# Optimization experiments

Hardware: AMD Instinct MI355X
Metric: run time of the kernel (lower is better)

Reference implementation:

```python
import jax, jax.numpy as jnp
import numpy as np

INPUT_SIZE = 768
HIDDEN = 384


def _gru_dir(x, W_ih, W_hh, b_ih, b_hh, reverse):
    """Single-direction GRU, torch gate order (r, z, n).
    x: [B, S, D] -> outputs [B, S, H]."""
    B = x.shape[0]
    H = W_hh.shape[1]
    # Precompute input projections for all timesteps: [B, S, 3H] -> [S, B, 3H]
    xw = jnp.swapaxes(x @ W_ih.T + b_ih, 0, 1)

    def step(h, xw_t):
        gh = h @ W_hh.T + b_hh
        xr, xz, xn = jnp.split(xw_t, 3, axis=-1)
        hr, hz, hn = jnp.split(gh, 3, axis=-1)
        r = jax.nn.sigmoid(xr + hr)
        z = jax.nn.sigmoid(xz + hz)
        n = jnp.tanh(xn + r * hn)
        h_new = (1.0 - z) * n + z * h
        return h_new, h_new

    h0 = jnp.zeros((B, H), dtype=x.dtype)
    _, hs = jax.lax.scan(step, h0, xw, reverse=reverse)  # [S, B, H]
    return jnp.swapaxes(hs, 0, 1)


def setup_inputs() -> dict:
    key = jax.random.key(0)
    ks = jax.random.split(key, 12)
    B, S, D, H = 32, 512, INPUT_SIZE, HIDDEN
    s_ih = 1.0 / np.sqrt(H)
    u = lambda k, shape: jax.random.uniform(k, shape, jnp.float32, -s_ih, s_ih)
    inp = {
        "ip": jax.random.normal(ks[0], (B, S, D), jnp.float32),
        # forward-direction GRU params
        "W_ih_f": u(ks[1], (3 * H, D)),
        "W_hh_f": u(ks[2], (3 * H, H)),
        "b_ih_f": u(ks[3], (3 * H,)),
        "b_hh_f": u(ks[4], (3 * H,)),
        # backward-direction GRU params
        "W_ih_b": u(ks[5], (3 * H, D)),
        "W_hh_b": u(ks[6], (3 * H, H)),
        "b_ih_b": u(ks[7], (3 * H,)),
        "b_hh_b": u(ks[8], (3 * H,)),
        # sentence attention params (input_dim = 2H)
        "W_attn": u(ks[9], (2 * H, 2 * H)),
        "b_attn": u(ks[10], (2 * H,)),
        "context": jax.random.normal(ks[11], (2 * H,), jnp.float32) * 0.05,
    }
    return inp


def reference(ip, W_ih_f, W_hh_f, b_ih_f, b_hh_f,
              W_ih_b, W_hh_b, b_ih_b, b_hh_b,
              W_attn, b_attn, context):
    # BiGRU encode: concat forward & backward hidden states -> [B, S, 2H]
    h_f = _gru_dir(ip, W_ih_f, W_hh_f, b_ih_f, b_hh_f, reverse=False)
    h_b = _gru_dir(ip, W_ih_b, W_hh_b, b_ih_b, b_hh_b, reverse=True)
    out = jnp.concatenate([h_f, h_b], axis=-1)
    # Additive attention pooling over sentences
    scores = jnp.tanh(out @ W_attn.T + b_attn) @ context  # [B, S]
    attn = jax.nn.softmax(scores, axis=1)
    doc_embeds = jnp.einsum("bs,bsd->bd", attn, out)  # [B, 2H]
    return doc_embeds
```

## Files before the change

kernel.cpp:

```cpp
#include <hip/hip_runtime.h>
#include <hip/hip_fp16.h>

typedef _Float16 half2_t __attribute__((ext_vector_type(2)));
typedef _Float16 half4_t __attribute__((ext_vector_type(4)));
typedef _Float16 half8_t __attribute__((ext_vector_type(8)));
typedef float floatx4 __attribute__((ext_vector_type(4)));

#define B_   32
#define S_   512
#define D_   768
#define H_   384
#define H3_  1152
#define M_   (B_*S_)
#define N2_  (2*H3_)
#define TWOH_ 768
#define NWG_DIR 6
#define JSPAN 64

__device__ __forceinline__ int4 load16_cc(const void* p) {
  int4 r;
  unsigned long long a = (unsigned long long)p;
  asm volatile("global_load_dwordx4 %0, %1, off sc0 sc1\n\t"
               "s_waitcnt vmcnt(0)"
               : "=v"(r) : "v"(a) : "memory");
  return r;
}
__device__ __forceinline__ void load16_cc3(const void* p0, const void* p1, const void* p2,
                                           int4& v0, int4& v1, int4& v2) {
  unsigned long long a0 = (unsigned long long)p0;
  unsigned long long a1 = (unsigned long long)p1;
  unsigned long long a2 = (unsigned long long)p2;
  asm volatile("global_load_dwordx4 %0, %3, off sc0 sc1\n\t"
               "global_load_dwordx4 %1, %4, off sc0 sc1\n\t"
               "global_load_dwordx4 %2, %5, off sc0 sc1\n\t"
               "s_waitcnt vmcnt(0)"
               : "=&v"(v0), "=&v"(v1), "=&v"(v2)
               : "v"(a0), "v"(a1), "v"(a2) : "memory");
}
__device__ __forceinline__ void store8_cc(void* p, int2 v) {
  unsigned long long a = (unsigned long long)p;
  asm volatile("global_store_dwordx2 %0, %1, off sc0 sc1"
               :: "v"(a), "v"(v) : "memory");
}
__device__ __forceinline__ void wait_vm0() {
  asm volatile("s_waitcnt vmcnt(0)" ::: "memory");
}

__global__ void cvt_f32_f16_kernel(const float* __restrict__ src,
                                   _Float16* __restrict__ dst, int n4) {
  int i = blockIdx.x * blockDim.x + threadIdx.x;
  if (i >= n4) return;
  float4 v = ((const float4*)src)[i];
  half4_t h = {(_Float16)v.x, (_Float16)v.y, (_Float16)v.z, (_Float16)v.w};
  ((half4_t*)dst)[i] = h;
}

__global__ __launch_bounds__(256) void gemm_xw_kernel(
    const _Float16* __restrict__ A, const _Float16* __restrict__ Bm,
    const float* __restrict__ bias_f, const float* __restrict__ bias_b,
    _Float16* __restrict__ xw) {
  __shared__ _Float16 As[64][40];
  __shared__ _Float16 Bs[64][40];
  const int m0 = blockIdx.x * 64, n0 = blockIdx.y * 64;
  const int tid = threadIdx.x, lane = tid & 63, w = tid >> 6;
  const int wm = w >> 1, wn = w & 1;
  const int q = lane >> 4, c = lane & 15;
  floatx4 acc[2][2] = {};

  const int t = tid & 127;
  const int srow = t >> 1, skh = (t & 1) * 16;
  const _Float16* gsrc =
      (tid < 128 ? A + (size_t)(m0 + srow) * D_ : Bm + (size_t)(n0 + srow) * D_) + skh;
  _Float16* ldst = (tid < 128) ? &As[srow][skh] : &Bs[srow][skh];

  for (int k0 = 0; k0 < D_; k0 += 32) {
    half8_t v0 = *(const half8_t*)(gsrc + k0);
    half8_t v1 = *(const half8_t*)(gsrc + k0 + 8);
    __syncthreads();
    *(half8_t*)ldst = v0;
    *(half8_t*)(ldst + 8) = v1;
    __syncthreads();
    half8_t a0 = *(const half8_t*)&As[wm * 32 + c][q * 8];
    half8_t a1 = *(const half8_t*)&As[wm * 32 + 16 + c][q * 8];
    half8_t b0 = *(const half8_t*)&Bs[wn * 32 + c][q * 8];
    half8_t b1 = *(const half8_t*)&Bs[wn * 32 + 16 + c][q * 8];
    acc[0][0] = __builtin_amdgcn_mfma_f32_16x16x32_f16(a0, b0, acc[0][0], 0, 0, 0);
    acc[0][1] = __builtin_amdgcn_mfma_f32_16x16x32_f16(a0, b1, acc[0][1], 0, 0, 0);
    acc[1][0] = __builtin_amdgcn_mfma_f32_16x16x32_f16(a1, b0, acc[1][0], 0, 0, 0);
    acc[1][1] = __builtin_amdgcn_mfma_f32_16x16x32_f16(a1, b1, acc[1][1], 0, 0, 0);
  }
  for (int mi = 0; mi < 2; ++mi)
    for (int ni = 0; ni < 2; ++ni)
      for (int r = 0; r < 4; ++r) {
        int m = m0 + wm * 32 + mi * 16 + q * 4 + r;
        int n = n0 + wn * 32 + ni * 16 + c;
        int dir = n >= H3_;
        int nn = n - dir * H3_;
        float bv = dir ? bias_b[nn] : bias_f[nn];
        float vv = acc[mi][ni][r] + bv;
        int s = m & (S_ - 1), bb = m >> 9;
        xw[(((size_t)dir * S_ + s) * B_ + bb) * H3_ + nn] = (_Float16)vv;
      }
}

__global__ __launch_bounds__(512, 2) void gru_mfma_kernel(
    const _Float16* __restrict__ xw,
    const _Float16* __restrict__ Whh,
    const float* __restrict__ bhh_f, const float* __restrict__ bhh_b,
    _Float16* __restrict__ hglob,
    _Float16* __restrict__ out16,
    int* __restrict__ bar) {
  const int wg = blockIdx.x;
  const int dir = wg / NWG_DIR;
  const int wgj = wg % NWG_DIR;
  const int j0w = wgj * JSPAN;
  const int tid = threadIdx.x, lane = tid & 63, w = tid >> 6;
  const int bt = w & 1, jt = w >> 1;
  const int c = lane & 15, q = lane >> 4;

  __shared__ __align__(16) _Float16 hS[32 * 392];
  __shared__ __align__(16) float ghS[3 * 32 * 68];

  half8_t bfr[3][12];
  {
    const int jglob = j0w + jt * 16 + c;
#pragma unroll
    for (int g = 0; g < 3; ++g) {
      const _Float16* wp = Whh + ((size_t)dir * H3_ + g * H_ + jglob) * H_ + q * 8;
#pragma unroll
      for (int kt = 0; kt < 12; ++kt) bfr[g][kt] = *(const half8_t*)(wp + kt * 32);
    }
  }
  const float* bhh = dir ? bhh_b : bhh_f;
  const int gb = tid >> 4, jq = tid & 15;
  const int jg4 = j0w + jq * 4;
  float br[4], bz[4], bn[4], hc[4];
#pragma unroll
  for (int i = 0; i < 4; ++i) {
    br[i] = bhh[jg4 + i];
    bz[i] = bhh[H_ + jg4 + i];
    bn[i] = bhh[2 * H_ + jg4 + i];
    hc[i] = 0.f;
  }
  int* flg = bar + dir * 256;

  for (int step = 0; step < S_; ++step) {
    const int t = dir ? (S_ - 1 - step) : step;
    const int par = step & 1;

    const _Float16* xp = xw + (((size_t)dir * S_ + t) * B_ + gb) * H3_ + jg4;
    half4_t xr4 = *(const half4_t*)(xp);
    half4_t xz4 = *(const half4_t*)(xp + H_);
    half4_t xn4 = *(const half4_t*)(xp + 2 * H_);

    if (step > 0 && w == 0) {
      int v;
      do {
        v = (lane < NWG_DIR)
                ? __hip_atomic_load(&flg[lane * 16], __ATOMIC_RELAXED,
                                    __HIP_MEMORY_SCOPE_AGENT)
                : 0x7fffffff;
      } while (!__all(v >= step));
    }
    __syncthreads();

    {
      const _Float16* hb = hglob + ((size_t)dir * 2 + par) * B_ * H_;
      int g0 = tid, g1 = tid + 512, g2 = tid + 1024;
      int4 v0, v1, v2;
      load16_cc3(hb + (g0 / 48) * H_ + (g0 % 48) * 8,
                 hb + (g1 / 48) * H_ + (g1 % 48) * 8,
                 hb + (g2 / 48) * H_ + (g2 % 48) * 8, v0, v1, v2);
      *(int4*)&hS[(g0 / 48) * 392 + (g0 % 48) * 8] = v0;
      *(int4*)&hS[(g1 / 48) * 392 + (g1 % 48) * 8] = v1;
      *(int4*)&hS[(g2 / 48) * 392 + (g2 % 48) * 8] = v2;
    }
    __syncthreads();

    floatx4 a0 = {}, a1 = {}, a2 = {};
    {
      const _Float16* hrow = &hS[(bt * 16 + c) * 392 + q * 8];
#pragma unroll
      for (int kt = 0; kt < 12; ++kt) {
        half8_t af = *(const half8_t*)(hrow + kt * 32);
        a0 = __builtin_amdgcn_mfma_f32_16x16x32_f16(af, bfr[0][kt], a0, 0, 0, 0);
        a1 = __builtin_amdgcn_mfma_f32_16x16x32_f16(af, bfr[1][kt], a1, 0, 0, 0);
        a2 = __builtin_amdgcn_mfma_f32_16x16x32_f16(af, bfr[2][kt], a2, 0, 0, 0);
      }
    }
#pragma unroll
    for (int r = 0; r < 4; ++r) {
      int brow = bt * 16 + q * 4 + r;
      ghS[(0 * 32 + brow) * 68 + jt * 16 + c] = a0[r];
      ghS[(1 * 32 + brow) * 68 + jt * 16 + c] = a1[r];
      ghS[(2 * 32 + brow) * 68 + jt * 16 + c] = a2[r];
    }
    __syncthreads();

    floatx4 arv = *(floatx4*)&ghS[(0 * 32 + gb) * 68 + jq * 4];
    floatx4 azv = *(floatx4*)&ghS[(1 * 32 + gb) * 68 + jq * 4];
    floatx4 anv = *(floatx4*)&ghS[(2 * 32 + gb) * 68 + jq * 4];
    half4_t hh;
#pragma unroll
    for (int i = 0; i < 4; ++i) {
      float rr = 1.f / (1.f + __expf(-((float)xr4[i] + arv[i] + br[i])));
      float zz = 1.f / (1.f + __expf(-((float)xz4[i] + azv[i] + bz[i])));
      float u = (float)xn4[i] + rr * (anv[i] + bn[i]);
      float e = __expf(-2.f * u);
      float nv = (1.f - e) / (1.f + e);
      hc[i] = (1.f - zz) * nv + zz * hc[i];
      hh[i] = (_Float16)hc[i];
    }
    store8_cc(hglob + (((size_t)dir * 2 + (par ^ 1)) * B_ + gb) * H_ + jg4,
              __builtin_bit_cast(int2, hh));
    wait_vm0();
    __syncthreads();
    if (tid == 0)
      __hip_atomic_store(&flg[wgj * 16], step + 1, __ATOMIC_RELAXED,
                         __HIP_MEMORY_SCOPE_AGENT);
    *(half4_t*)&out16[((size_t)gb * S_ + t) * TWOH_ + dir * H_ + jg4] = hh;
  }
}

__global__ __launch_bounds__(256) void attn_score_kernel(
    const _Float16* __restrict__ A ,
    const _Float16* __restrict__ Bm ,
    const float* __restrict__ b_attn, const float* __restrict__ ctx,
    float* __restrict__ scores) {
  __shared__ _Float16 As[64][40];
  __shared__ _Float16 Bs[64][40];
  const int m0 = blockIdx.x * 64, n0 = blockIdx.y * 64;
  const int tid = threadIdx.x, lane = tid & 63, w = tid >> 6;
  const int wm = w >> 1, wn = w & 1;
  const int q = lane >> 4, c = lane & 15;
  floatx4 acc[2][2] = {};

  const int t = tid & 127;
  const int srow = t >> 1, skh = (t & 1) * 16;
  const _Float16* gsrc =
      (tid < 128 ? A + (size_t)(m0 + srow) * D_ : Bm + (size_t)(n0 + srow) * D_) + skh;
  _Float16* ldst = (tid < 128) ? &As[srow][skh] : &Bs[srow][skh];

  for (int k0 = 0; k0 < D_; k0 += 32) {
    half8_t v0 = *(const half8_t*)(gsrc + k0);
    half8_t v1 = *(const half8_t*)(gsrc + k0 + 8);
    __syncthreads();
    *(half8_t*)ldst = v0;
    *(half8_t*)(ldst + 8) = v1;
    __syncthreads();
    half8_t a0 = *(const half8_t*)&As[wm * 32 + c][q * 8];
    half8_t a1 = *(const half8_t*)&As[wm * 32 + 16 + c][q * 8];
    half8_t b0 = *(const half8_t*)&Bs[wn * 32 + c][q * 8];
    half8_t b1 = *(const half8_t*)&Bs[wn * 32 + 16 + c][q * 8];
    acc[0][0] = __builtin_amdgcn_mfma_f32_16x16x32_f16(a0, b0, acc[0][0], 0, 0, 0);
    acc[0][1] = __builtin_amdgcn_mfma_f32_16x16x32_f16(a0, b1, acc[0][1], 0, 0, 0);
    acc[1][0] = __builtin_amdgcn_mfma_f32_16x16x32_f16(a1, b0, acc[1][0], 0, 0, 0);
    acc[1][1] = __builtin_amdgcn_mfma_f32_16x16x32_f16(a1, b1, acc[1][1], 0, 0, 0);
  }
  for (int mi = 0; mi < 2; ++mi)
    for (int ni = 0; ni < 2; ++ni)
      for (int r = 0; r < 4; ++r) {
        int n = n0 + wn * 32 + ni * 16 + c;
        float vv = tanhf(acc[mi][ni][r] + b_attn[n]) * ctx[n];
        vv += __shfl_xor(vv, 1);
        vv += __shfl_xor(vv, 2);
        vv += __shfl_xor(vv, 4);
        vv += __shfl_xor(vv, 8);
        if (c == 0) {
          int m = m0 + wm * 32 + mi * 16 + q * 4 + r;
          atomicAdd(&scores[m], vv);
        }
      }
}

__global__ __launch_bounds__(256) void softmax_kernel(const float* __restrict__ scores,
                                                      float* __restrict__ attn) {
  const int b = blockIdx.x, tid = threadIdx.x;
  __shared__ float red[8];
  float s0 = scores[b * S_ + tid], s1 = scores[b * S_ + 256 + tid];
  float m = fmaxf(s0, s1);
  for (int off = 1; off < 64; off <<= 1) m = fmaxf(m, __shfl_xor(m, off));
  int wv = tid >> 6;
  if ((tid & 63) == 0) red[wv] = m;
  __syncthreads();
  m = fmaxf(fmaxf(red[0], red[1]), fmaxf(red[2], red[3]));
  float e0 = expf(s0 - m), e1 = expf(s1 - m);
  float sum = e0 + e1;
  for (int off = 1; off < 64; off <<= 1) sum += __shfl_xor(sum, off);
  if ((tid & 63) == 0) red[4 + wv] = sum;
  __syncthreads();
  sum = red[4] + red[5] + red[6] + red[7];
  float inv = 1.0f / sum;
  attn[b * S_ + tid] = e0 * inv;
  attn[b * S_ + 256 + tid] = e1 * inv;
}

__global__ __launch_bounds__(384) void doc_kernel(const float* __restrict__ attn,
                                                  const _Float16* __restrict__ out16,
                                                  float* __restrict__ dout) {
  const int b = blockIdx.x, tid = threadIdx.x;
  __shared__ float at[S_];
  for (int i = tid; i < S_; i += 384) at[i] = attn[b * S_ + i];
  __syncthreads();
  const half2_t* p = (const half2_t*)(out16 + (size_t)b * S_ * TWOH_) + tid;
  float acc0 = 0.f, acc1 = 0.f;
  for (int s = 0; s < S_; ++s) {
    half2_t h = p[(size_t)s * (TWOH_ / 2)];
    float wgt = at[s];
    acc0 += wgt * (float)h.x;
    acc1 += wgt * (float)h.y;
  }
  dout[b * TWOH_ + tid * 2] = acc0;
  dout[b * TWOH_ + tid * 2 + 1] = acc1;
}

extern "C" void kernel_launch(void* const* d_in, const int* in_sizes, int n_in,
                              void* d_out, int out_size, void* d_ws, size_t ws_size,
                              hipStream_t stream) {
  const float* ip     = (const float*)d_in[0];
  const float* W_ih_f = (const float*)d_in[1];
  const float* W_hh_f = (const float*)d_in[2];
  const float* b_ih_f = (const float*)d_in[3];
  const float* b_hh_f_p = (const float*)d_in[4];
  const float* W_ih_b = (const float*)d_in[5];
  const float* W_hh_b = (const float*)d_in[6];
  const float* b_ih_b = (const float*)d_in[7];
  const float* b_hh_b_p = (const float*)d_in[8];
  const float* W_attn = (const float*)d_in[9];
  const float* b_attn = (const float*)d_in[10];
  const float* context = (const float*)d_in[11];
  float* doc = (float*)d_out;

  char* ws = (char*)d_ws;
  size_t off = 0;
  auto alloc = [&](size_t bytes) {
    char* p = ws + off;
    off += (bytes + 255) & ~(size_t)255;
    return p;
  };
  _Float16* ip16    = (_Float16*)alloc((size_t)M_ * D_ * 2);
  _Float16* Wih16   = (_Float16*)alloc((size_t)N2_ * D_ * 2);
  _Float16* Whh16   = (_Float16*)alloc((size_t)2 * H3_ * H_ * 2);
  _Float16* Wattn16 = (_Float16*)alloc((size_t)TWOH_ * TWOH_ * 2);
  _Float16* xw      = (_Float16*)alloc((size_t)2 * S_ * B_ * H3_ * 2);
  _Float16* out16   = (_Float16*)alloc((size_t)B_ * S_ * TWOH_ * 2);
  _Float16* hglob   = (_Float16*)alloc((size_t)2 * 2 * B_ * H_ * 2);
  int*      bar     = (int*)alloc(4096);
  float* scores     = (float*)alloc((size_t)M_ * 4);
  float* attn       = (float*)alloc((size_t)M_ * 4);

  cvt_f32_f16_kernel<<<(M_ * D_ / 4 + 255) / 256, 256, 0, stream>>>(ip, ip16, M_ * D_ / 4);
  cvt_f32_f16_kernel<<<(H3_ * D_ / 4 + 255) / 256, 256, 0, stream>>>(W_ih_f, Wih16, H3_ * D_ / 4);
  cvt_f32_f16_kernel<<<(H3_ * D_ / 4 + 255) / 256, 256, 0, stream>>>(W_ih_b, Wih16 + (size_t)H3_ * D_, H3_ * D_ / 4);
  cvt_f32_f16_kernel<<<(H3_ * H_ / 4 + 255) / 256, 256, 0, stream>>>(W_hh_f, Whh16, H3_ * H_ / 4);
  cvt_f32_f16_kernel<<<(H3_ * H_ / 4 + 255) / 256, 256, 0, stream>>>(W_hh_b, Whh16 + (size_t)H3_ * H_, H3_ * H_ / 4);
  cvt_f32_f16_kernel<<<(TWOH_ * TWOH_ / 4 + 255) / 256, 256, 0, stream>>>(W_attn, Wattn16, TWOH_ * TWOH_ / 4);

  gemm_xw_kernel<<<dim3(M_ / 64, N2_ / 64), 256, 0, stream>>>(ip16, Wih16, b_ih_f, b_ih_b, xw);

  hipMemsetAsync(hglob, 0, (size_t)2 * 2 * B_ * H_ * 2, stream);
  hipMemsetAsync(bar, 0, 4096, stream);
  {
    const _Float16* xw_a = xw;
    const _Float16* whh_a = Whh16;
    const float* bf_a = b_hh_f_p;
    const float* bb_a = b_hh_b_p;
    _Float16* hg_a = hglob;
    _Float16* o16_a = out16;
    int* bar_a = bar;
    void* args[] = {(void*)&xw_a, (void*)&whh_a, (void*)&bf_a, (void*)&bb_a,
                    (void*)&hg_a, (void*)&o16_a, (void*)&bar_a};
    hipLaunchCooperativeKernel((const void*)gru_mfma_kernel, dim3(2 * NWG_DIR),
                               dim3(512), args, 0, stream);
  }

  hipMemsetAsync(scores, 0, (size_t)M_ * 4, stream);
  attn_score_kernel<<<dim3(M_ / 64, TWOH_ / 64), 256, 0, stream>>>(out16, Wattn16, b_attn, context, scores);

  softmax_kernel<<<B_, 256, 0, stream>>>(scores, attn);
  doc_kernel<<<B_, 384, 0, stream>>>(attn, out16, doc);
}
```

Before: 2.169 ms.

## Replace GRU step barrier with step-tagged hidden-state words and in-register gate math

Replaces the per-step flag barrier between workgroups with a scheme where each hidden value is stored as a 32-bit word carrying the step number in its upper half. Consumers spin on reading the whole hidden state until every tag matches, which removes the separate flag poll, the store wait and two block barriers per step. The gate nonlinearity now runs directly on the MFMA accumulator registers instead of going through a shared-memory gh buffer, and hS is double-buffered. In exchange the global hidden state traffic doubles, stores become scattered 4-byte writes, and correctness depends on the 32-bit tagged writes being observed atomically.

```diff
diff --git a/kernel.cpp b/kernel.cpp
--- a/kernel.cpp
+++ b/kernel.cpp
@@ -17,33 +17,24 @@
 #define NWG_DIR 6
 #define JSPAN 64
 
-__device__ __forceinline__ int4 load16_cc(const void* p) {
-  int4 r;
-  unsigned long long a = (unsigned long long)p;
-  asm volatile("global_load_dwordx4 %0, %1, off sc0 sc1\n\t"
+__device__ __forceinline__ void load16_cc6(unsigned long long a0, unsigned long long a1,
+                                           unsigned long long a2, unsigned long long a3,
+                                           unsigned long long a4, unsigned long long a5,
+                                           int4& v0, int4& v1, int4& v2,
+                                           int4& v3, int4& v4, int4& v5) {
+  asm volatile("global_load_dwordx4 %0, %6, off sc0 sc1\n\t"
+               "global_load_dwordx4 %1, %7, off sc0 sc1\n\t"
+               "global_load_dwordx4 %2, %8, off sc0 sc1\n\t"
+               "global_load_dwordx4 %3, %9, off sc0 sc1\n\t"
+               "global_load_dwordx4 %4, %10, off sc0 sc1\n\t"
+               "global_load_dwordx4 %5, %11, off sc0 sc1\n\t"
                "s_waitcnt vmcnt(0)"
-               : "=v"(r) : "v"(a) : "memory");
-  return r;
-}
-__device__ __forceinline__ void load16_cc3(const void* p0, const void* p1, const void* p2,
-                                           int4& v0, int4& v1, int4& v2) {
-  unsigned long long a0 = (unsigned long long)p0;
-  unsigned long long a1 = (unsigned long long)p1;
-  unsigned long long a2 = (unsigned long long)p2;
-  asm volatile("global_load_dwordx4 %0, %3, off sc0 sc1\n\t"
-               "global_load_dwordx4 %1, %4, off sc0 sc1\n\t"
-               "global_load_dwordx4 %2, %5, off sc0 sc1\n\t"
-               "s_waitcnt vmcnt(0)"
-               : "=&v"(v0), "=&v"(v1), "=&v"(v2)
-               : "v"(a0), "v"(a1), "v"(a2) : "memory");
-}
-__device__ __forceinline__ void store8_cc(void* p, int2 v) {
-  unsigned long long a = (unsigned long long)p;
-  asm volatile("global_store_dwordx2 %0, %1, off sc0 sc1"
-               :: "v"(a), "v"(v) : "memory");
-}
-__device__ __forceinline__ void wait_vm0() {
-  asm volatile("s_waitcnt vmcnt(0)" ::: "memory");
+               : "=&v"(v0), "=&v"(v1), "=&v"(v2), "=&v"(v3), "=&v"(v4), "=&v"(v5)
+               : "v"(a0), "v"(a1), "v"(a2), "v"(a3), "v"(a4), "v"(a5)
+               : "memory");
+}
+__device__ __forceinline__ void store4_cc(unsigned long long a, unsigned d) {
+  asm volatile("global_store_dword %0, %1, off sc0 sc1" :: "v"(a), "v"(d) : "memory");
 }
 
 __global__ void cvt_f32_f16_kernel(const float* __restrict__ src,
@@ -107,9 +98,8 @@
     const _Float16* __restrict__ xw,
     const _Float16* __restrict__ Whh,
     const float* __restrict__ bhh_f, const float* __restrict__ bhh_b,
-    _Float16* __restrict__ hglob,
-    _Float16* __restrict__ out16,
-    int* __restrict__ bar) {
+    unsigned* __restrict__ hT,
+    _Float16* __restrict__ out16) {
   const int wg = blockIdx.x;
   const int dir = wg / NWG_DIR;
   const int wgj = wg % NWG_DIR;
@@ -118,8 +108,7 @@
   const int bt = w & 1, jt = w >> 1;
   const int c = lane & 15, q = lane >> 4;
 
-  __shared__ __align__(16) _Float16 hS[32 * 392];
-  __shared__ __align__(16) float ghS[3 * 32 * 68];
+  __shared__ __align__(16) _Float16 hS[2][32 * 392];
 
   half8_t bfr[3][12];
   {
@@ -132,54 +121,63 @@
     }
   }
   const float* bhh = dir ? bhh_b : bhh_f;
-  const int gb = tid >> 4, jq = tid & 15;
-  const int jg4 = j0w + jq * 4;
-  float br[4], bz[4], bn[4], hc[4];
-#pragma unroll
-  for (int i = 0; i < 4; ++i) {
-    br[i] = bhh[jg4 + i];
-    bz[i] = bhh[H_ + jg4 + i];
-    bn[i] = bhh[2 * H_ + jg4 + i];
-    hc[i] = 0.f;
-  }
-  int* flg = bar + dir * 256;
+  const int jl = j0w + jt * 16 + c;
+  const int bl0 = bt * 16 + q * 4;
+  const float br = bhh[jl], bz = bhh[H_ + jl], bn = bhh[2 * H_ + jl];
+  float hc[4] = {0.f, 0.f, 0.f, 0.f};
+
+  unsigned* const hTd = hT + (size_t)dir * 2 * B_ * H_;
 
   for (int step = 0; step < S_; ++step) {
     const int t = dir ? (S_ - 1 - step) : step;
     const int par = step & 1;
 
-    const _Float16* xp = xw + (((size_t)dir * S_ + t) * B_ + gb) * H3_ + jg4;
-    half4_t xr4 = *(const half4_t*)(xp);
-    half4_t xz4 = *(const half4_t*)(xp + H_);
-    half4_t xn4 = *(const half4_t*)(xp + 2 * H_);
-
-    if (step > 0 && w == 0) {
-      int v;
-      do {
-        v = (lane < NWG_DIR)
-                ? __hip_atomic_load(&flg[lane * 16], __ATOMIC_RELAXED,
-                                    __HIP_MEMORY_SCOPE_AGENT)
-                : 0x7fffffff;
-      } while (!__all(v >= step));
-    }
-    __syncthreads();
-
-    {
-      const _Float16* hb = hglob + ((size_t)dir * 2 + par) * B_ * H_;
-      int g0 = tid, g1 = tid + 512, g2 = tid + 1024;
-      int4 v0, v1, v2;
-      load16_cc3(hb + (g0 / 48) * H_ + (g0 % 48) * 8,
-                 hb + (g1 / 48) * H_ + (g1 % 48) * 8,
-                 hb + (g2 / 48) * H_ + (g2 % 48) * 8, v0, v1, v2);
-      *(int4*)&hS[(g0 / 48) * 392 + (g0 % 48) * 8] = v0;
-      *(int4*)&hS[(g1 / 48) * 392 + (g1 % 48) * 8] = v1;
-      *(int4*)&hS[(g2 / 48) * 392 + (g2 % 48) * 8] = v2;
+    const _Float16* xbase = xw + (((size_t)dir * S_ + t) * B_ + bl0) * H3_ + jl;
+    _Float16 xr[4], xz[4], xn[4];
+#pragma unroll
+    for (int r = 0; r < 4; ++r) {
+      xr[r] = xbase[(size_t)r * H3_];
+      xz[r] = xbase[(size_t)r * H3_ + H_];
+      xn[r] = xbase[(size_t)r * H3_ + 2 * H_];
+    }
+
+    _Float16* hcur = &hS[par][0];
+    if (step == 0) {
+      for (int i = tid; i < 32 * 392 / 2; i += 512) ((int*)hcur)[i] = 0;
+    } else {
+      const unsigned long long a =
+          (unsigned long long)(hTd + (size_t)par * (B_ * H_)) + (size_t)tid * 16;
+      const unsigned tg = (unsigned)step;
+      int4 v0, v1, v2, v3, v4, v5;
+      for (;;) {
+        load16_cc6(a, a + 8192, a + 16384, a + 24576, a + 32768, a + 40960,
+                   v0, v1, v2, v3, v4, v5);
+#define TAGCHK(v) ((((unsigned)(v).x >> 16) ^ tg) | (((unsigned)(v).y >> 16) ^ tg) | \
+                   (((unsigned)(v).z >> 16) ^ tg) | (((unsigned)(v).w >> 16) ^ tg))
+        unsigned bad = TAGCHK(v0) | TAGCHK(v1) | TAGCHK(v2) |
+                       TAGCHK(v3) | TAGCHK(v4) | TAGCHK(v5);
+#undef TAGCHK
+        if (bad == 0) break;
+      }
+      {
+        const int4 vv[6] = {v0, v1, v2, v3, v4, v5};
+#pragma unroll
+        for (int k = 0; k < 6; ++k) {
+          int g = tid + (k << 9);
+          int b = g / 96;
+          int cj = g - b * 96;
+          int2 wds;
+          wds.x = (vv[k].x & 0xffff) | ((unsigned)vv[k].y << 16);
+          wds.y = (vv[k].z & 0xffff) | ((unsigned)vv[k].w << 16);
+          *(int2*)&hcur[b * 392 + cj * 4] = wds;
+        }
+      }
     }
     __syncthreads();
 
     floatx4 a0 = {}, a1 = {}, a2 = {};
     {
-      const _Float16* hrow = &hS[(bt * 16 + c) * 392 + q * 8];
+      const _Float16* hrow = &hcur[(bt * 16 + c) * 392 + q * 8];
 #pragma unroll
       for (int kt = 0; kt < 12; ++kt) {
         half8_t af = *(const half8_t*)(hrow + kt * 32);
@@ -188,37 +186,22 @@
         a2 = __builtin_amdgcn_mfma_f32_16x16x32_f16(af, bfr[2][kt], a2, 0, 0, 0);
       }
     }
+
+    const unsigned tagw = (unsigned)(step + 1) << 16;
+    unsigned* hdst = hTd + ((size_t)((step + 1) & 1) * B_ + bl0) * H_ + jl;
 #pragma unroll
     for (int r = 0; r < 4; ++r) {
-      int brow = bt * 16 + q * 4 + r;
-      ghS[(0 * 32 + brow) * 68 + jt * 16 + c] = a0[r];
-      ghS[(1 * 32 + brow) * 68 + jt * 16 + c] = a1[r];
-      ghS[(2 * 32 + brow) * 68 + jt * 16 + c] = a2[r];
-    }
-    __syncthreads();
-
-    floatx4 arv = *(floatx4*)&ghS[(0 * 32 + gb) * 68 + jq * 4];
-    floatx4 azv = *(floatx4*)&ghS[(1 * 32 + gb) * 68 + jq * 4];
-    floatx4 anv = *(floatx4*)&ghS[(2 * 32 + gb) * 68 + jq * 4];
-    half4_t hh;
-#pragma unroll
-    for (int i = 0; i < 4; ++i) {
-      float rr = 1.f / (1.f + __expf(-((float)xr4[i] + arv[i] + br[i])));
-      float zz = 1.f / (1.f + __expf(-((float)xz4[i] + azv[i] + bz[i])));
-      float u = (float)xn4[i] + rr * (anv[i] + bn[i]);
+      float rr = 1.f / (1.f + __expf(-((float)xr[r] + a0[r] + br)));
+      float zz = 1.f / (1.f + __expf(-((float)xz[r] + a1[r] + bz)));
+      float u = (float)xn[r] + rr * (a2[r] + bn);
       float e = __expf(-2.f * u);
       float nv = (1.f - e) / (1.f + e);
-      hc[i] = (1.f - zz) * nv + zz * hc[i];
-      hh[i] = (_Float16)hc[i];
-    }
-    store8_cc(hglob + (((size_t)dir * 2 + (par ^ 1)) * B_ + gb) * H_ + jg4,
-              __builtin_bit_cast(int2, hh));
-    wait_vm0();
-    __syncthreads();
-    if (tid == 0)
-      __hip_atomic_store(&flg[wgj * 16], step + 1, __ATOMIC_RELAXED,
-                         __HIP_MEMORY_SCOPE_AGENT);
-    *(half4_t*)&out16[((size_t)gb * S_ + t) * TWOH_ + dir * H_ + jg4] = hh;
+      hc[r] = (1.f - zz) * nv + zz * hc[r];
+      _Float16 hh = (_Float16)hc[r];
+      unsigned d = tagw | (unsigned)__builtin_bit_cast(unsigned short, hh);
+      store4_cc((unsigned long long)(hdst + (size_t)r * H_), d);
+      out16[((size_t)(bl0 + r) * S_ + t) * TWOH_ + dir * H_ + jl] = hh;
+    }
   }
 }
 
@@ -344,8 +327,7 @@
   _Float16* Wattn16 = (_Float16*)alloc((size_t)TWOH_ * TWOH_ * 2);
   _Float16* xw      = (_Float16*)alloc((size_t)2 * S_ * B_ * H3_ * 2);
   _Float16* out16   = (_Float16*)alloc((size_t)B_ * S_ * TWOH_ * 2);
-  _Float16* hglob   = (_Float16*)alloc((size_t)2 * 2 * B_ * H_ * 2);
-  int*      bar     = (int*)alloc(4096);
+  unsigned* hT      = (unsigned*)alloc((size_t)2 * 2 * B_ * H_ * 4);
   float* scores     = (float*)alloc((size_t)M_ * 4);
   float* attn       = (float*)alloc((size_t)M_ * 4);
 
@@ -358,18 +340,16 @@
 
   gemm_xw_kernel<<<dim3(M_ / 64, N2_ / 64), 256, 0, stream>>>(ip16, Wih16, b_ih_f, b_ih_b, xw);
 
-  hipMemsetAsync(hglob, 0, (size_t)2 * 2 * B_ * H_ * 2, stream);
-  hipMemsetAsync(bar, 0, 4096, stream);
+  hipMemsetAsync(hT, 0, (size_t)2 * 2 * B_ * H_ * 4, stream);
   {
     const _Float16* xw_a = xw;
     const _Float16* whh_a = Whh16;
     const float* bf_a = b_hh_f_p;
     const float* bb_a = b_hh_b_p;
-    _Float16* hg_a = hglob;
+    unsigned* ht_a = hT;
     _Float16* o16_a = out16;
-    int* bar_a = bar;
     void* args[] = {(void*)&xw_a, (void*)&whh_a, (void*)&bf_a, (void*)&bb_a,
-                    (void*)&hg_a, (void*)&o16_a, (void*)&bar_a};
+                    (void*)&ht_a, (void*)&o16_a};
     hipLaunchCooperativeKernel((const void*)gru_mfma_kernel, dim3(2 * NWG_DIR),
                                dim3(512), args, 0, stream);
   }
```

After: 2.444 ms. 12.7% more time.

## Apply GRU gates directly in MFMA registers with per-wave flags

Applied to the files above, without the earlier changes.

The gate nonlinearities are now computed directly from the MFMA accumulator registers. This removes the shared-memory ghS round trip and the __syncthreads around it. Cross-workgroup synchronisation moves from one flag per workgroup set by thread 0 after a barrier to one flag per wave, which every wave polls with a 16-byte coherent load, so the final block-wide barrier goes away. In exchange, hidden-state stores shrink to 2-byte scattered writes and xw loads become scalar halves, and there are more flags to poll. The step-0 path zero-fills shared memory instead of reading the hidden state.

```diff
diff --git a/kernel.cpp b/kernel.cpp
--- a/kernel.cpp
+++ b/kernel.cpp
@@ -37,10 +37,14 @@
                : "=&v"(v0), "=&v"(v1), "=&v"(v2)
                : "v"(a0), "v"(a1), "v"(a2) : "memory");
 }
-__device__ __forceinline__ void store8_cc(void* p, int2 v) {
+__device__ __forceinline__ void store2_cc(void* p, unsigned short v) {
   unsigned long long a = (unsigned long long)p;
-  asm volatile("global_store_dwordx2 %0, %1, off sc0 sc1"
-               :: "v"(a), "v"(v) : "memory");
+  unsigned d = v;
+  asm volatile("global_store_short %0, %1, off sc0 sc1" :: "v"(a), "v"(d) : "memory");
+}
+__device__ __forceinline__ void store4_cc(void* p, int d) {
+  unsigned long long a = (unsigned long long)p;
+  asm volatile("global_store_dword %0, %1, off sc0 sc1" :: "v"(a), "v"(d) : "memory");
 }
 __device__ __forceinline__ void wait_vm0() {
   asm volatile("s_waitcnt vmcnt(0)" ::: "memory");
@@ -103,7 +107,7 @@
       }
 }
 
-__global__ __launch_bounds__(512, 2) void gru_mfma_kernel(
+__global__ __launch_bounds__(512, 1) void gru_mfma_kernel(
     const _Float16* __restrict__ xw,
     const _Float16* __restrict__ Whh,
     const float* __restrict__ bhh_f, const float* __restrict__ bhh_b,
@@ -119,7 +123,6 @@
   const int c = lane & 15, q = lane >> 4;
 
   __shared__ __align__(16) _Float16 hS[32 * 392];
-  __shared__ __align__(16) float ghS[3 * 32 * 68];
 
   half8_t bfr[3][12];
   {
@@ -132,39 +135,37 @@
     }
   }
   const float* bhh = dir ? bhh_b : bhh_f;
-  const int gb = tid >> 4, jq = tid & 15;
-  const int jg4 = j0w + jq * 4;
-  float br[4], bz[4], bn[4], hc[4];
-#pragma unroll
-  for (int i = 0; i < 4; ++i) {
-    br[i] = bhh[jg4 + i];
-    bz[i] = bhh[H_ + jg4 + i];
-    bn[i] = bhh[2 * H_ + jg4 + i];
-    hc[i] = 0.f;
-  }
-  int* flg = bar + dir * 256;
+  const int jl = j0w + jt * 16 + c;
+  const int bl0 = bt * 16 + q * 4;
+  const float br = bhh[jl], bz = bhh[H_ + jl], bn = bhh[2 * H_ + jl];
+  float hc[4] = {0.f, 0.f, 0.f, 0.f};
+
+  int* const flg = bar + dir * 64;
+  const int fw = wgj * 8 + w;
+  const int* fpoll = flg + ((lane < 12) ? lane * 4 : 0);
 
   for (int step = 0; step < S_; ++step) {
     const int t = dir ? (S_ - 1 - step) : step;
     const int par = step & 1;
 
-    const _Float16* xp = xw + (((size_t)dir * S_ + t) * B_ + gb) * H3_ + jg4;
-    half4_t xr4 = *(const half4_t*)(xp);
-    half4_t xz4 = *(const half4_t*)(xp + H_);
-    half4_t xn4 = *(const half4_t*)(xp + 2 * H_);
-
-    if (step > 0 && w == 0) {
-      int v;
-      do {
-        v = (lane < NWG_DIR)
-                ? __hip_atomic_load(&flg[lane * 16], __ATOMIC_RELAXED,
-                                    __HIP_MEMORY_SCOPE_AGENT)
-                : 0x7fffffff;
-      } while (!__all(v >= step));
-    }
-    __syncthreads();
-
-    {
+    const _Float16* xbase = xw + (((size_t)dir * S_ + t) * B_ + bl0) * H3_ + jl;
+    _Float16 xr[4], xz[4], xn[4];
+#pragma unroll
+    for (int r = 0; r < 4; ++r) {
+      xr[r] = xbase[(size_t)r * H3_];
+      xz[r] = xbase[(size_t)r * H3_ + H_];
+      xn[r] = xbase[(size_t)r * H3_ + 2 * H_];
+    }
+
+    if (step == 0) {
+      for (int i = tid; i < 32 * 392 / 2; i += 512) ((int*)hS)[i] = 0;
+    } else {
+      for (;;) {
+        int4 f = load16_cc(fpoll);
+        bool ok = (lane >= 12) ||
+                  (f.x >= step && f.y >= step && f.z >= step && f.w >= step);
+        if (__all(ok)) break;
+      }
       const _Float16* hb = hglob + ((size_t)dir * 2 + par) * B_ * H_;
       int g0 = tid, g1 = tid + 512, g2 = tid + 1024;
       int4 v0, v1, v2;
@@ -188,37 +189,27 @@
         a2 = __builtin_amdgcn_mfma_f32_16x16x32_f16(af, bfr[2][kt], a2, 0, 0, 0);
       }
     }
+
+    _Float16* hdst = hglob + ((size_t)dir * 2 + (par ^ 1)) * B_ * H_ +
+                     (size_t)bl0 * H_ + jl;
+    _Float16 hh4[4];
 #pragma unroll
     for (int r = 0; r < 4; ++r) {
-      int brow = bt * 16 + q * 4 + r;
-      ghS[(0 * 32 + brow) * 68 + jt * 16 + c] = a0[r];
-      ghS[(1 * 32 + brow) * 68 + jt * 16 + c] = a1[r];
-      ghS[(2 * 32 + brow) * 68 + jt * 16 + c] = a2[r];
-    }
-    __syncthreads();
-
-    floatx4 arv = *(floatx4*)&ghS[(0 * 32 + gb) * 68 + jq * 4];
-    floatx4 azv = *(floatx4*)&ghS[(1 * 32 + gb) * 68 + jq * 4];
-    floatx4 anv = *(floatx4*)&ghS[(2 * 32 + gb) * 68 + jq * 4];
-    half4_t hh;
-#pragma unroll
-    for (int i = 0; i < 4; ++i) {
-      float rr = 1.f / (1.f + __expf(-((float)xr4[i] + arv[i] + br[i])));
-      float zz = 1.f / (1.f + __expf(-((float)xz4[i] + azv[i] + bz[i])));
-      float u = (float)xn4[i] + rr * (anv[i] + bn[i]);
+      float rr = 1.f / (1.f + __expf(-((float)xr[r] + a0[r] + br)));
+      float zz = 1.f / (1.f + __expf(-((float)xz[r] + a1[r] + bz)));
+      float u = (float)xn[r] + rr * (a2[r] + bn);
       float e = __expf(-2.f * u);
       float nv = (1.f - e) / (1.f + e);
-      hc[i] = (1.f - zz) * nv + zz * hc[i];
-      hh[i] = (_Float16)hc[i];
-    }
-    store8_cc(hglob + (((size_t)dir * 2 + (par ^ 1)) * B_ + gb) * H_ + jg4,
-              __builtin_bit_cast(int2, hh));
+      hc[r] = (1.f - zz) * nv + zz * hc[r];
+      hh4[r] = (_Float16)hc[r];
+      store2_cc(hdst + (size_t)r * H_,
+                __builtin_bit_cast(unsigned short, hh4[r]));
+    }
     wait_vm0();
-    __syncthreads();
-    if (tid == 0)
-      __hip_atomic_store(&flg[wgj * 16], step + 1, __ATOMIC_RELAXED,
-                         __HIP_MEMORY_SCOPE_AGENT);
-    *(half4_t*)&out16[((size_t)gb * S_ + t) * TWOH_ + dir * H_ + jg4] = hh;
+    if (lane == 0) store4_cc(flg + fw, step + 1);
+#pragma unroll
+    for (int r = 0; r < 4; ++r)
+      out16[((size_t)(bl0 + r) * S_ + t) * TWOH_ + dir * H_ + jl] = hh4[r];
   }
 }
 
```

Result: slower. 2.471 ms (+13.9%).
